# Optimization experiments

Measured on AMD Instinct MI355X. Metric: run time of the kernel, lower is better.

The kernel has to match this reference:

```python
import jax, jax.numpy as jnp
import numpy as np

N_NODES = 50000
N_EDGES = 800000
N_ITERS = 7
D_H = 128      # n_node_features (GRU hidden)
D_IN = 64      # n_node_inputs
D_EDGE = 128   # n_edge_features
D_OUT = 64     # n_node_outputs
MLP_H = 96     # hardcoded msg_net hidden


def setup_inputs() -> dict:
    key = jax.random.key(0)
    ks = jax.random.split(key, 16)
    s = 0.05
    return {
        "node_inputs": jax.random.normal(ks[0], (N_NODES, D_IN), dtype=jnp.float32),
        "src_ids": jax.random.randint(ks[1], (N_EDGES,), 0, N_NODES),
        "dst_ids": jax.random.randint(ks[2], (N_EDGES,), 0, N_NODES),
        "W1": jax.random.normal(ks[3], (MLP_H, 2 * D_H), dtype=jnp.float32) * s,
        "b1": jax.random.normal(ks[4], (MLP_H,), dtype=jnp.float32) * s,
        "W2": jax.random.normal(ks[5], (MLP_H, MLP_H), dtype=jnp.float32) * s,
        "b2": jax.random.normal(ks[6], (MLP_H,), dtype=jnp.float32) * s,
        "W3": jax.random.normal(ks[7], (D_EDGE, MLP_H), dtype=jnp.float32) * s,
        "b3": jax.random.normal(ks[8], (D_EDGE,), dtype=jnp.float32) * s,
        "W_ih": jax.random.normal(ks[9], (3 * D_H, D_IN + D_EDGE), dtype=jnp.float32) * s,
        "W_hh": jax.random.normal(ks[10], (3 * D_H, D_H), dtype=jnp.float32) * s,
        "b_ih": jax.random.normal(ks[11], (3 * D_H,), dtype=jnp.float32) * s,
        "b_hh": jax.random.normal(ks[12], (3 * D_H,), dtype=jnp.float32) * s,
        "W_out": jax.random.normal(ks[13], (D_OUT, D_H), dtype=jnp.float32) * s,
        "b_out": jax.random.normal(ks[14], (D_OUT,), dtype=jnp.float32) * s,
    }


def reference(node_inputs, src_ids, dst_ids, W1, b1, W2, b2, W3, b3,
              W_ih, W_hh, b_ih, b_hh, W_out, b_out):
    n_nodes = node_inputs.shape[0]
    d_h = W_hh.shape[1]

    def step(h, _):
        # gather -> message MLP over edges
        m = jnp.concatenate([h[src_ids], h[dst_ids]], axis=1)   # [E, 2*d_h]
        m = jax.nn.relu(m @ W1.T + b1)
        m = jax.nn.relu(m @ W2.T + b2)
        m = m @ W3.T + b3                                        # [E, d_edge]
        # scatter-add to destination nodes (index_add_)
        agg = jax.ops.segment_sum(m, dst_ids, num_segments=n_nodes)
        # GRU cell (PyTorch gate ordering: r, z, n)
        x = jnp.concatenate([node_inputs, agg], axis=1)          # [N, d_in+d_edge]
        gi = x @ W_ih.T + b_ih
        gh = h @ W_hh.T + b_hh
        i_r, i_z, i_n = jnp.split(gi, 3, axis=1)
        h_r, h_z, h_n = jnp.split(gh, 3, axis=1)
        r = jax.nn.sigmoid(i_r + h_r)
        z = jax.nn.sigmoid(i_z + h_z)
        n = jnp.tanh(i_n + r * h_n)
        h_new = (1.0 - z) * n + z * h
        out = h_new @ W_out.T + b_out                            # [N, d_out]
        return h_new, out

    h0 = jnp.zeros((n_nodes, d_h), dtype=node_inputs.dtype)
    _, outputs = jax.lax.scan(step, h0, None, length=N_ITERS)
    return outputs  # [n_iters, n_nodes, n_node_outputs]
```

## Files before the change

kernel.cpp:

```cpp
#include <hip/hip_runtime.h>

#define N_NODES 50000
#define N_EDGES 800000
#define N_ITERS 7
#define NPAD 50048
#define NT16 (N_EDGES / 16)
#define TOTP 1024
#define TPP ((NT16 + TOTP - 1) / TOTP)

typedef __attribute__((ext_vector_type(8))) short short8;
typedef __attribute__((ext_vector_type(4))) float f32x4;

#define AROW 104
#define XROW 296

static __device__ __forceinline__ unsigned short f2bf(float f) {
    unsigned int u = __float_as_uint(f);
    unsigned int r = (u + 0x7fffu + ((u >> 16) & 1u)) >> 16;
    return (unsigned short)r;
}
static __device__ __forceinline__ float bf2f(unsigned short u) {
    return __uint_as_float(((unsigned int)u) << 16);
}
static __device__ __forceinline__ unsigned cvt_pk_bf16(float lo, float hi) {
    unsigned r;
    asm("v_cvt_pk_bf16_f32 %0, %1, %2" : "=v"(r) : "v"(lo), "v"(hi));
    return r;
}
static __device__ __forceinline__ float fast_tanh(float x) {
    float xc = fminf(fmaxf(x, -15.f), 15.f);
    float t = __expf(2.f * xc);
    return (t - 1.f) / (t + 1.f);
}
static __device__ __forceinline__ float ror_prev(float x) {
    return __int_as_float(__builtin_amdgcn_update_dpp(0, __float_as_int(x), 0x121, 0xf, 0xf, true));
}

template <int CTRL, int N>
static __device__ __forceinline__ void seg_step(float (&s)[N], unsigned& fl) {
    unsigned fv = (unsigned)__builtin_amdgcn_update_dpp(0, (int)fl, CTRL, 0xf, 0xf, true);
    float g = fl ? 0.f : 1.f;
#pragma unroll
    for (int q = 0; q < N; q++) {
        int sv = __builtin_amdgcn_update_dpp(0, __float_as_int(s[q]), CTRL, 0xf, 0xf, true);
        s[q] += __int_as_float(sv) * g;
    }
    fl |= fv;
}

__global__ __launch_bounds__(256) void k_build_wbig(const float* __restrict__ W_ih,
                                                    const float* __restrict__ W3,
                                                    const float* __restrict__ W_hh,
                                                    float* __restrict__ Wbig) {
    int idx = blockIdx.x * 256 + threadIdx.x;
    if (idx >= 256 * 288) return;
    int g = idx / 288, k = idx - g * 288;
    float v;
    if (k < 64) v = W_ih[g * 192 + k];
    else if (k < 160) {
        int kk = k - 64; float s = 0.f;
        for (int j = 0; j < 128; j++) s += W_ih[g * 192 + 64 + j] * W3[j * 96 + kk];
        v = s;
    } else v = W_hh[g * 128 + (k - 160)];
    Wbig[idx] = v;
}

__global__ __launch_bounds__(256) void k_build_wni(const float* __restrict__ W_ih,
                                                   const float* __restrict__ W3,
                                                   float* __restrict__ Wni) {
    int idx = blockIdx.x * 256 + threadIdx.x;
    if (idx >= 128 * 160) return;
    int g = idx / 160, k = idx - g * 160;
    int gg = 256 + g;
    float v;
    if (k < 64) v = W_ih[gg * 192 + k];
    else {
        int kk = k - 64; float s = 0.f;
        for (int j = 0; j < 128; j++) s += W_ih[gg * 192 + 64 + j] * W3[j * 96 + kk];
        v = s;
    }
    Wni[idx] = v;
}

__global__ __launch_bounds__(256) void k_vb3(const float* __restrict__ W_ih,
                                             const float* __restrict__ b3,
                                             float* __restrict__ vb3) {
    int g = blockIdx.x * 256 + threadIdx.x;
    if (g >= 384) return;
    float s = 0.f;
    for (int j = 0; j < 128; j++) s += W_ih[g * 192 + 64 + j] * b3[j];
    vb3[g] = s;
}

__global__ __launch_bounds__(256) void k_bsum(const float* __restrict__ b_ih,
                                              const float* __restrict__ b_hh,
                                              float* __restrict__ bsum) {
    int d = blockIdx.x * 256 + threadIdx.x;
    if (d >= 384) return;
    bsum[d] = b_ih[d] + (d < 256 ? b_hh[d] : 0.f);
}

__global__ __launch_bounds__(256) void k_pack2(const float* __restrict__ src,
                                               unsigned short* __restrict__ out,
                                               int Mt, int KT, int ld, int row0) {
    int idx = blockIdx.x * 256 + threadIdx.x;
    if (idx >= Mt * KT * 512) return;
    int jj = idx & 7;
    int l  = (idx >> 3) & 63;
    int tile = idx >> 9;
    int kt = tile % KT;
    int mt = tile / KT;
    int j = row0 + mt * 16 + (l & 15);
    int k = kt * 32 + (l >> 4) * 8 + jj;
    out[idx] = f2bf(src[(size_t)j * ld + k]);
}

__global__ __launch_bounds__(256) void k_hist(const int* __restrict__ dst,
                                              int* __restrict__ counts) {
    int e = blockIdx.x * 256 + threadIdx.x;
    if (e < N_EDGES) atomicAdd(&counts[dst[e]], 1);
}

__global__ __launch_bounds__(1024) void k_scan(const int* __restrict__ counts,
                                               int* __restrict__ row_off) {
    __shared__ int sh[1024];
    int t = threadIdx.x;
    const int STR = 49;
    int base = t * STR;
    int s = 0;
    for (int i = 0; i < STR; i++) {
        int n = base + i;
        if (n < N_NODES) s += counts[n];
    }
    sh[t] = s;
    __syncthreads();
    for (int off = 1; off < 1024; off <<= 1) {
        int v = (t >= off) ? sh[t - off] : 0;
        __syncthreads();
        sh[t] += v;
        __syncthreads();
    }
    int run = (t == 0) ? 0 : sh[t - 1];
    for (int i = 0; i < STR; i++) {
        int n = base + i;
        if (n < N_NODES) { row_off[n] = run; run += counts[n]; }
    }
    if (t == 1023) row_off[N_NODES] = run;
}

__global__ __launch_bounds__(256) void k_permute(const int* __restrict__ src,
                                                 const int* __restrict__ dst,
                                                 const int* __restrict__ row_off,
                                                 int* __restrict__ cursor,
                                                 int* __restrict__ perm_src,
                                                 int* __restrict__ perm_dst) {
    int e = blockIdx.x * 256 + threadIdx.x;
    if (e >= N_EDGES) return;
    int d = dst[e];
    int pos = row_off[d] + atomicAdd(&cursor[d], 1);
    perm_src[pos] = src[e];
    perm_dst[pos] = d;
}

__global__ __launch_bounds__(256) void k_edge_fused(
    const unsigned short* __restrict__ hbf,
    const int* __restrict__ perm_src, const int* __restrict__ perm_dst,
    const short8* __restrict__ W1Ag,
    const short8* __restrict__ W2Ag,
    const float* __restrict__ b1,
    const float* __restrict__ b2,
    float* __restrict__ r2agg)
{
    __shared__ __attribute__((aligned(16))) short8 W1s[6 * 8 * 64];
    __shared__ __attribute__((aligned(16))) short8 W2s[6 * 3 * 64];
    __shared__ __attribute__((aligned(16))) unsigned short relay[2][16][AROW];

    int t = threadIdx.x;
    int w = t >> 6, l = t & 63;
    int col = l & 15, krow = l >> 4;
    int pair = w >> 1;
    int u = w & 1;
    int mtb = 3 * u;

    for (int i = t; i < 6 * 8 * 64; i += 256) W1s[i] = W1Ag[i];
    for (int i = t; i < 6 * 3 * 64; i += 256) W2s[i] = W2Ag[i];
    __syncthreads();

    int pidx = blockIdx.x * 2 + pair;
    int tlo = pidx * TPP;
    int thi = tlo + TPP; if (thi > NT16) thi = NT16;
    int ntiles = thi - tlo; if (ntiles < 0) ntiles = 0;

    float carry[12];
#pragma unroll
    for (int q = 0; q < 12; q++) carry[q] = 0.f;
    bool head = true;

    int te0 = tlo; if (te0 >= NT16) te0 = NT16 - 1;
    int sid, did;
    { int e = te0 * 16 + col; sid = perm_src[e]; did = perm_dst[e]; }
    short8 frS[4], frD[4];
    {
        const unsigned short* sr = hbf + (size_t)sid * 128 + krow * 8;
        const unsigned short* dr = hbf + (size_t)did * 128 + krow * 8;
#pragma unroll
        for (int kt = 0; kt < 4; kt++) frS[kt] = *(const short8*)(sr + kt * 32);
#pragma unroll
        for (int kt = 0; kt < 4; kt++) frD[kt] = *(const short8*)(dr + kt * 32);
    }

    for (int tt = 0; tt < TPP; ++tt) {
        bool active = (tt < ntiles);
        bool hasN = (tt + 1 < ntiles);
        int teN = tlo + tt + 1; if (teN >= NT16) teN = NT16 - 1;
        int sidN, didN;
        { int e = teN * 16 + col; sidN = perm_src[e]; didN = perm_dst[e]; }

        int dp = __shfl_up(did, 1);
        unsigned m16 = (unsigned)__ballot((col == 0) || (did != dp)) & 0xFFFFu;
        bool continuing = hasN && (__shfl(did, 15) == __shfl(didN, 0));

        f32x4 c1[3] = {};
        __builtin_amdgcn_s_setprio(1);
#pragma unroll
        for (int kt = 0; kt < 4; kt++) {
#pragma unroll
            for (int mt = 0; mt < 3; mt++)
                c1[mt] = __builtin_amdgcn_mfma_f32_16x16x32_bf16(W1s[((mtb + mt) * 8 + kt) * 64 + l], frS[kt], c1[mt], 0, 0, 0);
        }
#pragma unroll
        for (int kt = 0; kt < 4; kt++) {
#pragma unroll
            for (int mt = 0; mt < 3; mt++)
                c1[mt] = __builtin_amdgcn_mfma_f32_16x16x32_bf16(W1s[((mtb + mt) * 8 + 4 + kt) * 64 + l], frD[kt], c1[mt], 0, 0, 0);
        }
        __builtin_amdgcn_s_setprio(0);

#pragma unroll
        for (int mt = 0; mt < 3; mt++) {
#pragma unroll
            for (int r = 0; r < 4; r += 2) {
                int j0 = (mtb + mt) * 16 + krow * 4 + r;
                float v0 = fmaxf(c1[mt][r]     + b1[j0],     0.f);
                float v1 = fmaxf(c1[mt][r + 1] + b1[j0 + 1], 0.f);
                *(unsigned int*)(&relay[pair][col][j0]) = cvt_pk_bf16(v0, v1);
            }
        }
        __syncthreads();

        {
            const unsigned short* sr = hbf + (size_t)sidN * 128 + krow * 8;
            const unsigned short* dr = hbf + (size_t)didN * 128 + krow * 8;
#pragma unroll
            for (int kt = 0; kt < 4; kt++) frS[kt] = *(const short8*)(sr + kt * 32);
#pragma unroll
            for (int kt = 0; kt < 4; kt++) frD[kt] = *(const short8*)(dr + kt * 32);
        }

        f32x4 c2[3] = {};
        __builtin_amdgcn_s_setprio(1);
#pragma unroll
        for (int kt = 0; kt < 3; kt++) {
            short8 b = *(const short8*)(&relay[pair][col][kt * 32 + krow * 8]);
#pragma unroll
            for (int mt = 0; mt < 3; mt++)
                c2[mt] = __builtin_amdgcn_mfma_f32_16x16x32_bf16(W2s[((mtb + mt) * 3 + kt) * 64 + l], b, c2[mt], 0, 0, 0);
        }
        __builtin_amdgcn_s_setprio(0);

        float s[12];
#pragma unroll
        for (int mt = 0; mt < 3; mt++)
#pragma unroll
            for (int r = 0; r < 4; r++) {
                int j = (mtb + mt) * 16 + krow * 4 + r;
                float v = fmaxf(c2[mt][r] + b2[j], 0.f);
                s[mt * 4 + r] = v + ((col == 0) ? carry[mt * 4 + r] : 0.f);
            }
        unsigned fl = (m16 >> col) & 1u;
        seg_step<0x111>(s, fl);
        seg_step<0x112>(s, fl);
        seg_step<0x114>(s, fl);
        seg_step<0x118>(s, fl);
        bool is_end = (col == 15) || ((m16 >> (col + 1)) & 1u);
        if (active && is_end && !((col == 15) && continuing)) {
            unsigned lowmask = (2u << col) - 1u;
            bool first_seg = (__popc(m16 & lowmask) == 1);
            bool use_atomic = (first_seg && head) || ((col == 15) && !hasN);
            float* base = r2agg + (size_t)did * 96 + krow * 4;
            if (use_atomic) {
#pragma unroll
                for (int mt = 0; mt < 3; mt++)
#pragma unroll
                    for (int r = 0; r < 4; r++)
                        atomicAdd(base + (mtb + mt) * 16 + r, s[mt * 4 + r]);
            } else {
#pragma unroll
                for (int mt = 0; mt < 3; mt++)
                    *(float4*)(base + (mtb + mt) * 16) = make_float4(s[mt * 4], s[mt * 4 + 1],
                                                                    s[mt * 4 + 2], s[mt * 4 + 3]);
            }
        }
        if (continuing) {
            head = head && (m16 == 1u);
#pragma unroll
            for (int q = 0; q < 12; q++) carry[q] = ror_prev(s[q]);
        } else {
            head = false;
#pragma unroll
            for (int q = 0; q < 12; q++) carry[q] = 0.f;
        }
        __syncthreads();
        sid = sidN; did = didN;
    }
}

__global__ __launch_bounds__(256) void k_node_mfma(
    const float* __restrict__ inp,
    const float* __restrict__ r2agg,
    const int* __restrict__ row_off,
    float* __restrict__ h,
    unsigned short* __restrict__ hbf,
    const short8* __restrict__ WbigA,
    const short8* __restrict__ WniA,
    const short8* __restrict__ WnhA,
    const short8* __restrict__ WoutA,
    const float* __restrict__ vb3,
    const float* __restrict__ bsum,
    const float* __restrict__ b_hh,
    const float* __restrict__ b_out,
    float* __restrict__ out, int iter)
{
    __shared__ __attribute__((aligned(16))) unsigned short X[4][16][XROW];
    __shared__ float degs[64];
    int t = threadIdx.x;
    int w = t >> 6, l = t & 63;
    int nb = blockIdx.x * 64;
    int col = l & 15, krow = l >> 4;

    for (int idx = t; idx < 64 * 32; idx += 256) {
        int i = idx >> 5, kk = (idx & 31) << 1;
        int n = nb + i;
        float2 v = make_float2(0.f, 0.f);
        if (n < N_NODES) v = *(const float2*)(inp + (size_t)n * 64 + kk);
        *(unsigned int*)(&X[i >> 4][i & 15][kk]) = cvt_pk_bf16(v.x, v.y);
    }
    for (int idx = t; idx < 64 * 48; idx += 256) {
        int i = (int)((unsigned)idx / 48u), kp = idx - i * 48;
        int n = nb + i;
        float2 v = make_float2(0.f, 0.f);
        if (n < N_NODES) v = *(const float2*)(r2agg + (size_t)n * 96 + kp * 2);
        *(unsigned int*)(&X[i >> 4][i & 15][64 + kp * 2]) = cvt_pk_bf16(v.x, v.y);
    }
    for (int idx = t; idx < 64 * 16; idx += 256) {
        int i = idx >> 4, c = idx & 15;
        int n = nb + i;
        uint4 v = make_uint4(0, 0, 0, 0);
        if (n < N_NODES) v = ((const uint4*)(hbf + (size_t)n * 128))[c];
        *(uint4*)(&X[i >> 4][i & 15][160 + c * 8]) = v;
    }
    if (t < 64) {
        int n = nb + t;
        degs[t] = (n < N_NODES) ? (float)(row_off[n + 1] - row_off[n]) : 0.f;
    }
    __syncthreads();

    int mts[4] = {2 * w, 2 * w + 1, 8 + 2 * w, 9 + 2 * w};
    f32x4 cg[4][4] = {};
#pragma unroll 3
    for (int kt = 0; kt < 9; kt++) {
        short8 b[4];
#pragma unroll
        for (int bf = 0; bf < 4; bf++) b[bf] = *(const short8*)(&X[bf][col][kt * 32 + krow * 8]);
#pragma unroll
        for (int mi = 0; mi < 4; mi++) {
            short8 a = WbigA[(mts[mi] * 9 + kt) * 64 + l];
#pragma unroll
            for (int bf = 0; bf < 4; bf++)
                cg[mi][bf] = __builtin_amdgcn_mfma_f32_16x16x32_bf16(a, b[bf], cg[mi][bf], 0, 0, 0);
        }
    }
    f32x4 ci[2][4] = {};
#pragma unroll
    for (int kt = 0; kt < 5; kt++) {
        short8 b[4];
#pragma unroll
        for (int bf = 0; bf < 4; bf++) b[bf] = *(const short8*)(&X[bf][col][kt * 32 + krow * 8]);
#pragma unroll
        for (int mi = 0; mi < 2; mi++) {
            short8 a = WniA[((2 * w + mi) * 5 + kt) * 64 + l];
#pragma unroll
            for (int bf = 0; bf < 4; bf++)
                ci[mi][bf] = __builtin_amdgcn_mfma_f32_16x16x32_bf16(a, b[bf], ci[mi][bf], 0, 0, 0);
        }
    }
    f32x4 ch[2][4] = {};
#pragma unroll
    for (int kt = 0; kt < 4; kt++) {
        short8 b[4];
#pragma unroll
        for (int bf = 0; bf < 4; bf++) b[bf] = *(const short8*)(&X[bf][col][160 + kt * 32 + krow * 8]);
#pragma unroll
        for (int mi = 0; mi < 2; mi++) {
            short8 a = WnhA[((2 * w + mi) * 4 + kt) * 64 + l];
#pragma unroll
            for (int bf = 0; bf < 4; bf++)
                ch[mi][bf] = __builtin_amdgcn_mfma_f32_16x16x32_bf16(a, b[bf], ch[mi][bf], 0, 0, 0);
        }
    }
    __syncthreads();

#pragma unroll
    for (int mi = 0; mi < 2; mi++) {
        int d0 = w * 32 + mi * 16 + krow * 4;
        float4 bsr = *(const float4*)(bsum + d0);
        float4 bsz = *(const float4*)(bsum + 128 + d0);
        float4 bsn = *(const float4*)(bsum + 256 + d0);
        float4 vbr = *(const float4*)(vb3 + d0);
        float4 vbz = *(const float4*)(vb3 + 128 + d0);
        float4 vbn = *(const float4*)(vb3 + 256 + d0);
        float4 bhn = *(const float4*)(b_hh + 256 + d0);
        float bsrv[4] = {bsr.x, bsr.y, bsr.z, bsr.w};
        float bszv[4] = {bsz.x, bsz.y, bsz.z, bsz.w};
        float bsnv[4] = {bsn.x, bsn.y, bsn.z, bsn.w};
        float vbrv[4] = {vbr.x, vbr.y, vbr.z, vbr.w};
        float vbzv[4] = {vbz.x, vbz.y, vbz.z, vbz.w};
        float vbnv[4] = {vbn.x, vbn.y, vbn.z, vbn.w};
        float bhnv[4] = {bhn.x, bhn.y, bhn.z, bhn.w};
#pragma unroll
        for (int bf = 0; bf < 4; bf++) {
            int n = nb + bf * 16 + col;
            bool valid = (n < N_NODES);
            float deg = degs[bf * 16 + col];
            float4 ho = make_float4(0.f, 0.f, 0.f, 0.f);
            if (valid) ho = *(const float4*)(h + (size_t)n * 128 + d0);
            float hov[4] = {ho.x, ho.y, ho.z, ho.w};
            float hv[4];
#pragma unroll
            for (int r = 0; r < 4; r++) {
                float rp = cg[mi][bf][r]     + bsrv[r] + deg * vbrv[r];
                float zp = cg[2 + mi][bf][r] + bszv[r] + deg * vbzv[r];
                float ip = ci[mi][bf][r]     + bsnv[r] + deg * vbnv[r];
                float hp = ch[mi][bf][r]     + bhnv[r];
                float rg = 1.f / (1.f + __expf(-rp));
                float zg = 1.f / (1.f + __expf(-zp));
                float ng = fast_tanh(ip + rg * hp);
                hv[r] = (1.f - zg) * ng + zg * hov[r];
            }
            if (valid)
                *(float4*)(h + (size_t)n * 128 + d0) = make_float4(hv[0], hv[1], hv[2], hv[3]);
            *(unsigned int*)(&X[bf][col][160 + d0])     = cvt_pk_bf16(hv[0], hv[1]);
            *(unsigned int*)(&X[bf][col][160 + d0 + 2]) = cvt_pk_bf16(hv[2], hv[3]);
        }
    }
    __syncthreads();

    f32x4 co[4] = {};
#pragma unroll
    for (int kt = 0; kt < 4; kt++) {
        short8 a = WoutA[(w * 4 + kt) * 64 + l];
#pragma unroll
        for (int bf = 0; bf < 4; bf++) {
            short8 b = *(const short8*)(&X[bf][col][160 + kt * 32 + krow * 8]);
            co[bf] = __builtin_amdgcn_mfma_f32_16x16x32_bf16(a, b, co[bf], 0, 0, 0);
        }
    }
    {
        int o0 = w * 16 + krow * 4;
        float4 bo = *(const float4*)(b_out + o0);
#pragma unroll
        for (int bf = 0; bf < 4; bf++) {
            int n = nb + bf * 16 + col;
            if (n < N_NODES) {
                float* op = out + (size_t)iter * N_NODES * 64 + (size_t)n * 64 + o0;
                *(float4*)op = make_float4(co[bf][0] + bo.x, co[bf][1] + bo.y,
                                           co[bf][2] + bo.z, co[bf][3] + bo.w);
            }
        }
    }

    for (int idx = t; idx < 64 * 16; idx += 256) {
        int i = idx >> 4, c = idx & 15;
        int n2 = nb + i;
        if (n2 < N_NODES)
            ((uint4*)(hbf + (size_t)n2 * 128))[c] = *(const uint4*)(&X[i >> 4][i & 15][160 + c * 8]);
    }
}

extern "C" void kernel_launch(void* const* d_in, const int* in_sizes, int n_in,
                              void* d_out, int out_size, void* d_ws, size_t ws_size,
                              hipStream_t stream)
{
    const float* inp   = (const float*)d_in[0];
    const int*   src   = (const int*)d_in[1];
    const int*   dst   = (const int*)d_in[2];
    const float* W1    = (const float*)d_in[3];
    const float* b1    = (const float*)d_in[4];
    const float* W2    = (const float*)d_in[5];
    const float* b2    = (const float*)d_in[6];
    const float* W3    = (const float*)d_in[7];
    const float* b3    = (const float*)d_in[8];
    const float* W_ih  = (const float*)d_in[9];
    const float* W_hh  = (const float*)d_in[10];
    const float* b_ih  = (const float*)d_in[11];
    const float* b_hh  = (const float*)d_in[12];
    const float* W_out = (const float*)d_in[13];
    const float* b_out = (const float*)d_in[14];
    float* out = (float*)d_out;

    char* ws = (char*)d_ws;
    size_t off = 0;
    auto alloc = [&](size_t bytes) -> void* {
        void* p = ws + off;
        off += (bytes + 255) & ~(size_t)255;
        return p;
    };
    float* h       = (float*)alloc((size_t)N_NODES * 128 * 4);
    unsigned short* hbf = (unsigned short*)alloc((size_t)N_NODES * 128 * 2);
    float* r2agg   = (float*)alloc((size_t)NPAD * 96 * 4);
    float* Wbig    = (float*)alloc((size_t)256 * 288 * 4);
    float* Wni     = (float*)alloc((size_t)128 * 160 * 4);
    float* vb3     = (float*)alloc((size_t)384 * 4);
    float* bsum    = (float*)alloc((size_t)384 * 4);
    unsigned short* W1A   = (unsigned short*)alloc((size_t)6 * 8 * 512 * 2);
    unsigned short* W2A   = (unsigned short*)alloc((size_t)6 * 3 * 512 * 2);
    unsigned short* WbigA = (unsigned short*)alloc((size_t)16 * 9 * 512 * 2);
    unsigned short* WniA  = (unsigned short*)alloc((size_t)8 * 5 * 512 * 2);
    unsigned short* WnhA  = (unsigned short*)alloc((size_t)8 * 4 * 512 * 2);
    unsigned short* WoutA = (unsigned short*)alloc((size_t)4 * 4 * 512 * 2);
    int*   counts  = (int*)alloc((size_t)N_NODES * 4);
    int*   cursor  = (int*)alloc((size_t)N_NODES * 4);
    int*   row_off = (int*)alloc((size_t)(N_NODES + 1) * 4);
    int*   perm_src= (int*)alloc((size_t)N_EDGES * 4);
    int*   perm_dst= (int*)alloc((size_t)N_EDGES * 4);

    hipMemsetAsync(h, 0, (size_t)N_NODES * 128 * 4, stream);
    hipMemsetAsync(hbf, 0, (size_t)N_NODES * 128 * 2, stream);
    hipMemsetAsync(counts, 0, (size_t)N_NODES * 4, stream);
    hipMemsetAsync(cursor, 0, (size_t)N_NODES * 4, stream);

    k_build_wbig<<<(256 * 288 + 255) / 256, 256, 0, stream>>>(W_ih, W3, W_hh, Wbig);
    k_build_wni<<<(128 * 160 + 255) / 256, 256, 0, stream>>>(W_ih, W3, Wni);
    k_vb3<<<2, 256, 0, stream>>>(W_ih, b3, vb3);
    k_bsum<<<2, 256, 0, stream>>>(b_ih, b_hh, bsum);

    k_pack2<<<(6 * 8 * 512 + 255) / 256, 256, 0, stream>>>(W1, W1A, 6, 8, 256, 0);
    k_pack2<<<(6 * 3 * 512 + 255) / 256, 256, 0, stream>>>(W2, W2A, 6, 3, 96, 0);
    k_pack2<<<(16 * 9 * 512 + 255) / 256, 256, 0, stream>>>(Wbig, WbigA, 16, 9, 288, 0);
    k_pack2<<<(8 * 5 * 512 + 255) / 256, 256, 0, stream>>>(Wni, WniA, 8, 5, 160, 0);
    k_pack2<<<(8 * 4 * 512 + 255) / 256, 256, 0, stream>>>(W_hh, WnhA, 8, 4, 128, 256);
    k_pack2<<<(4 * 4 * 512 + 255) / 256, 256, 0, stream>>>(W_out, WoutA, 4, 4, 128, 0);

    k_hist<<<(N_EDGES + 255) / 256, 256, 0, stream>>>(dst, counts);
    k_scan<<<1, 1024, 0, stream>>>(counts, row_off);
    k_permute<<<(N_EDGES + 255) / 256, 256, 0, stream>>>(src, dst, row_off, cursor,
                                                         perm_src, perm_dst);

    for (int it = 0; it < N_ITERS; ++it) {
        hipMemsetAsync(r2agg, 0, (size_t)NPAD * 96 * 4, stream);
        k_edge_fused<<<512, 256, 0, stream>>>(hbf, perm_src, perm_dst,
                                              (const short8*)W1A, (const short8*)W2A,
                                              b1, b2, r2agg);
        k_node_mfma<<<(N_NODES + 63) / 64, 256, 0, stream>>>(inp, r2agg, row_off, h, hbf,
                                                     (const short8*)WbigA, (const short8*)WniA,
                                                     (const short8*)WnhA, (const short8*)WoutA,
                                                     vb3, bsum, b_hh, b_out, out, it);
    }
}
```

Before: 1.660 ms.

## Double-buffer relay LDS, prefetch edge ids two tiles ahead, drop trailing barrier

The relay shared buffer is doubled so consecutive tiles alternate buffers, which lets the second __syncthreads per tile be removed. Edge index loads are moved two tiles ahead, and the next tile's h-fragment gathers are issued right after the first MFMA stage instead of after the barrier. The aim is to hide gather latency and cut barrier stalls, at the cost of more registers and LDS.

```diff
diff --git a/kernel.cpp b/kernel.cpp
--- a/kernel.cpp
+++ b/kernel.cpp
@@ -173,7 +173,7 @@
 {
     __shared__ __attribute__((aligned(16))) short8 W1s[6 * 8 * 64];
     __shared__ __attribute__((aligned(16))) short8 W2s[6 * 3 * 64];
-    __shared__ __attribute__((aligned(16))) unsigned short relay[2][16][AROW];
+    __shared__ __attribute__((aligned(16))) unsigned short relay[2][2][16][AROW];
 
     int t = threadIdx.x;
     int w = t >> 6, l = t & 63;
@@ -196,13 +196,17 @@
     for (int q = 0; q < 12; q++) carry[q] = 0.f;
     bool head = true;
 
-    int te0 = tlo; if (te0 >= NT16) te0 = NT16 - 1;
-    int sid, did;
-    { int e = te0 * 16 + col; sid = perm_src[e]; did = perm_dst[e]; }
+    auto ldids = [&](int tile, int& s_, int& d_) {
+        int te = tile; if (te >= NT16) te = NT16 - 1; if (te < 0) te = 0;
+        int e = te * 16 + col; s_ = perm_src[e]; d_ = perm_dst[e];
+    };
+    int sid0, did0, sid1, did1, sid2, did2;
+    ldids(tlo, sid0, did0);
+    ldids(tlo + 1, sid1, did1);
     short8 frS[4], frD[4];
     {
-        const unsigned short* sr = hbf + (size_t)sid * 128 + krow * 8;
-        const unsigned short* dr = hbf + (size_t)did * 128 + krow * 8;
+        const unsigned short* sr = hbf + (size_t)sid0 * 128 + krow * 8;
+        const unsigned short* dr = hbf + (size_t)did0 * 128 + krow * 8;
 #pragma unroll
         for (int kt = 0; kt < 4; kt++) frS[kt] = *(const short8*)(sr + kt * 32);
 #pragma unroll
@@ -212,13 +216,13 @@
     for (int tt = 0; tt < TPP; ++tt) {
         bool active = (tt < ntiles);
         bool hasN = (tt + 1 < ntiles);
-        int teN = tlo + tt + 1; if (teN >= NT16) teN = NT16 - 1;
-        int sidN, didN;
-        { int e = teN * 16 + col; sidN = perm_src[e]; didN = perm_dst[e]; }
-
-        int dp = __shfl_up(did, 1);
-        unsigned m16 = (unsigned)__ballot((col == 0) || (did != dp)) & 0xFFFFu;
-        bool continuing = hasN && (__shfl(did, 15) == __shfl(didN, 0));
+        int buf = tt & 1;
+
+        ldids(tlo + tt + 2, sid2, did2);
+
+        int dp = __shfl_up(did0, 1);
+        unsigned m16 = (unsigned)__ballot((col == 0) || (did0 != dp)) & 0xFFFFu;
+        bool continuing = hasN && (__shfl(did0, 15) == __shfl(did1, 0));
 
         f32x4 c1[3] = {};
         __builtin_amdgcn_s_setprio(1);
@@ -235,6 +239,15 @@
                 c1[mt] = __builtin_amdgcn_mfma_f32_16x16x32_bf16(W1s[((mtb + mt) * 8 + 4 + kt) * 64 + l], frD[kt], c1[mt], 0, 0, 0);
         }
         __builtin_amdgcn_s_setprio(0);
+
+        {
+            const unsigned short* sr = hbf + (size_t)sid1 * 128 + krow * 8;
+            const unsigned short* dr = hbf + (size_t)did1 * 128 + krow * 8;
+#pragma unroll
+            for (int kt = 0; kt < 4; kt++) frS[kt] = *(const short8*)(sr + kt * 32);
+#pragma unroll
+            for (int kt = 0; kt < 4; kt++) frD[kt] = *(const short8*)(dr + kt * 32);
+        }
 
 #pragma unroll
         for (int mt = 0; mt < 3; mt++) {
@@ -243,25 +256,16 @@
                 int j0 = (mtb + mt) * 16 + krow * 4 + r;
                 float v0 = fmaxf(c1[mt][r]     + b1[j0],     0.f);
                 float v1 = fmaxf(c1[mt][r + 1] + b1[j0 + 1], 0.f);
-                *(unsigned int*)(&relay[pair][col][j0]) = cvt_pk_bf16(v0, v1);
+                *(unsigned int*)(&relay[buf][pair][col][j0]) = cvt_pk_bf16(v0, v1);
             }
         }
         __syncthreads();
-
-        {
-            const unsigned short* sr = hbf + (size_t)sidN * 128 + krow * 8;
-            const unsigned short* dr = hbf + (size_t)didN * 128 + krow * 8;
-#pragma unroll
-            for (int kt = 0; kt < 4; kt++) frS[kt] = *(const short8*)(sr + kt * 32);
-#pragma unroll
-            for (int kt = 0; kt < 4; kt++) frD[kt] = *(const short8*)(dr + kt * 32);
-        }
 
         f32x4 c2[3] = {};
         __builtin_amdgcn_s_setprio(1);
 #pragma unroll
         for (int kt = 0; kt < 3; kt++) {
-            short8 b = *(const short8*)(&relay[pair][col][kt * 32 + krow * 8]);
+            short8 b = *(const short8*)(&relay[buf][pair][col][kt * 32 + krow * 8]);
 #pragma unroll
             for (int mt = 0; mt < 3; mt++)
                 c2[mt] = __builtin_amdgcn_mfma_f32_16x16x32_bf16(W2s[((mtb + mt) * 3 + kt) * 64 + l], b, c2[mt], 0, 0, 0);
@@ -287,7 +291,7 @@
             unsigned lowmask = (2u << col) - 1u;
             bool first_seg = (__popc(m16 & lowmask) == 1);
             bool use_atomic = (first_seg && head) || ((col == 15) && !hasN);
-            float* base = r2agg + (size_t)did * 96 + krow * 4;
+            float* base = r2agg + (size_t)did0 * 96 + krow * 4;
             if (use_atomic) {
 #pragma unroll
                 for (int mt = 0; mt < 3; mt++)
@@ -310,8 +314,8 @@
 #pragma unroll
             for (int q = 0; q < 12; q++) carry[q] = 0.f;
         }
-        __syncthreads();
-        sid = sidN; did = didN;
+        sid0 = sid1; did0 = did1;
+        sid1 = sid2; did1 = did2;
     }
 }
 
```

Result: faster. 1.581 ms (-4.7%).
